# Performance work log

Hardware: AMD Instinct MI355X
Metric: run time of the kernel (lower is better)

## Reference

```python
import jax, jax.numpy as jnp
import numpy as np

N = 50000          # nodes
E = 800000         # random edges (self loops added in forward)
F_IN = 64; F_HID = 64; F_OUT = 16; H = 2  # from layers=[64,64,64,16], heads=[2,2,2]
NEG_SLOPE = 0.2    # PyG GATConv default

def _glorot(key, shape):
    fan_in, fan_out = shape[0], shape[-1]
    lim = np.sqrt(6.0 / (fan_in + fan_out)).astype(np.float32)
    return jax.random.uniform(key, shape, jnp.float32, -lim, lim)

def gat_conv(x, src, dst, W, a_src, a_dst, b, concat):
    """PyG-style GATConv: gather -> attention logits -> segment softmax -> scatter-add."""
    n = x.shape[0]
    Hh, Ff = a_src.shape
    h = (x @ W).reshape(n, Hh, Ff)                      # [N,H,F]
    al_s = jnp.sum(h * a_src[None], axis=-1)            # [N,H]
    al_d = jnp.sum(h * a_dst[None], axis=-1)            # [N,H]
    e = jax.nn.leaky_relu(al_s[src] + al_d[dst], NEG_SLOPE)  # [Etot,H]
    emax = jax.ops.segment_max(e, dst, num_segments=n)       # [N,H]
    ex = jnp.exp(e - emax[dst])
    denom = jax.ops.segment_sum(ex, dst, num_segments=n)
    alpha = ex / (denom[dst] + 1e-16)                   # softmax over in-edges of dst
    out = jax.ops.segment_sum(h[src] * alpha[:, :, None], dst, num_segments=n)  # [N,H,F]
    out = out.reshape(n, Hh * Ff) if concat else out.mean(axis=1)
    return out + b

def setup_inputs() -> dict:
    key = jax.random.key(0)
    k = jax.random.split(key, 12)
    inp = {}
    inp["feat_matrix"] = jax.random.normal(k[0], (N, F_IN), jnp.float32)
    inp["edge_index"] = jax.random.randint(k[1], (2, E), 0, N, dtype=jnp.int32)
    inp["W1"] = _glorot(k[2], (F_IN, H * F_HID))
    inp["a1_src"] = _glorot(k[3], (H, F_HID)); inp["a1_dst"] = _glorot(k[4], (H, F_HID))
    inp["b1"] = jnp.zeros((H * F_HID,), jnp.float32)
    inp["W2"] = _glorot(k[5], (H * F_HID, H * F_HID))
    inp["a2_src"] = _glorot(k[6], (H, F_HID)); inp["a2_dst"] = _glorot(k[7], (H, F_HID))
    inp["b2"] = jnp.zeros((H * F_HID,), jnp.float32)
    inp["W3"] = _glorot(k[8], (H * F_HID, H * F_OUT))
    inp["a3_src"] = _glorot(k[9], (H, F_OUT)); inp["a3_dst"] = _glorot(k[10], (H, F_OUT))
    inp["b3"] = jnp.zeros((F_OUT,), jnp.float32)
    # unused forward args of the original module
    inp["get_item_index"] = 0; inp["set_index"] = 0; inp["val_index"] = 0; inp["mask_matrix"] = 0
    return inp

def reference(feat_matrix, edge_index, W1, a1_src, a1_dst, b1, W2, a2_src, a2_dst, b2,
              W3, a3_src, a3_dst, b3, get_item_index, set_index, val_index, mask_matrix):
    loops = jnp.arange(N, dtype=edge_index.dtype)
    src = jnp.concatenate([edge_index[0], loops])   # add_self_loops=True (PyG default)
    dst = jnp.concatenate([edge_index[1], loops])
    x = jax.nn.relu(gat_conv(feat_matrix, src, dst, W1, a1_src, a1_dst, b1, True))
    x = jax.nn.relu(gat_conv(x, src, dst, W2, a2_src, a2_dst, b2, True))
    x = gat_conv(x, src, dst, W3, a3_src, a3_dst, b3, False)
    return jax.nn.softmax(x, axis=-1)
```

## Files before the change

### kernel.cpp

```cpp
#include <hip/hip_runtime.h>
#include <hip/hip_fp16.h>

#define NEG_SLOPE 0.2f

__device__ __forceinline__ float lrelu(float x) { return x > 0.f ? x : NEG_SLOPE * x; }

template<int K, int OUT, int F, bool HSPLIT>
__global__ __launch_bounds__(256) void gemm_logits(
    const float* __restrict__ X, const float* __restrict__ W,
    const float* __restrict__ a_s, const float* __restrict__ a_d,
    float* __restrict__ HoutF, __half* __restrict__ HoutH,
    float* __restrict__ als, float* __restrict__ ald,
    int n)
{
    constexpr int TX = OUT / 4;
    constexpr int TY = 256 / TX;
    constexpr int MR = 8;
    constexpr int BM = TY * MR;
    constexpr int KC = 32;

    __shared__ __align__(16) float Xs[BM][KC];
    __shared__ __align__(16) float Ws[KC][OUT];

    const int tx = (int)threadIdx.x % TX;
    const int ty = (int)threadIdx.x / TX;
    const int r0 = blockIdx.x * BM;

    float4 acc[MR];
#pragma unroll
    for (int m = 0; m < MR; ++m) acc[m] = make_float4(0.f, 0.f, 0.f, 0.f);

    for (int kc = 0; kc < K; kc += KC) {
        __syncthreads();
        constexpr int XV = BM * KC / 4;
#pragma unroll
        for (int i = threadIdx.x; i < XV; i += 256) {
            int f = i * 4;
            int r = f / KC, k = f % KC;
            int gr = r0 + r;
            float4 v = make_float4(0.f, 0.f, 0.f, 0.f);
            if (gr < n) v = *(const float4*)(X + (size_t)gr * K + kc + k);
            *(float4*)(&Xs[r][k]) = v;
        }
        constexpr int WV = KC * OUT / 4;
#pragma unroll
        for (int i = threadIdx.x; i < WV; i += 256) {
            int f = i * 4;
            int k = f / OUT, c = f % OUT;
            *(float4*)(&Ws[k][c]) = *(const float4*)(W + (size_t)(kc + k) * OUT + c);
        }
        __syncthreads();

#pragma unroll
        for (int k4 = 0; k4 < KC; k4 += 4) {
            float4 xv[MR];
#pragma unroll
            for (int m = 0; m < MR; ++m)
                xv[m] = *(const float4*)(&Xs[ty * MR + m][k4]);
#pragma unroll
            for (int kk = 0; kk < 4; ++kk) {
                float4 wv = *(const float4*)(&Ws[k4 + kk][tx * 4]);
#pragma unroll
                for (int m = 0; m < MR; ++m) {
                    float xm = kk == 0 ? xv[m].x : kk == 1 ? xv[m].y : kk == 2 ? xv[m].z : xv[m].w;
                    acc[m].x = fmaf(xm, wv.x, acc[m].x);
                    acc[m].y = fmaf(xm, wv.y, acc[m].y);
                    acc[m].z = fmaf(xm, wv.z, acc[m].z);
                    acc[m].w = fmaf(xm, wv.w, acc[m].w);
                }
            }
        }
    }

    const float4 asv = *(const float4*)(a_s + tx * 4);
    const float4 adv = *(const float4*)(a_d + tx * 4);
    constexpr int UH = F / 4;
    const int head = tx / UH;
#pragma unroll
    for (int m = 0; m < MR; ++m) {
        int gr = r0 + ty * MR + m;
        float ps = acc[m].x * asv.x + acc[m].y * asv.y + acc[m].z * asv.z + acc[m].w * asv.w;
        float pd = acc[m].x * adv.x + acc[m].y * adv.y + acc[m].z * adv.z + acc[m].w * adv.w;
#pragma unroll
        for (int off = UH / 2; off > 0; off >>= 1) {
            ps += __shfl_xor(ps, off, 64);
            pd += __shfl_xor(pd, off, 64);
        }
        if (gr < n) {
            if (HSPLIT) {
                union { __half h[4]; uint2 u; } pk;
                pk.h[0] = __float2half_rn(acc[m].x);
                pk.h[1] = __float2half_rn(acc[m].y);
                pk.h[2] = __float2half_rn(acc[m].z);
                pk.h[3] = __float2half_rn(acc[m].w);
                *(uint2*)(HoutH + ((size_t)head * n + gr) * F + (tx % UH) * 4) = pk.u;
            } else {
                *(float4*)(HoutF + (size_t)gr * OUT + tx * 4) = acc[m];
            }
            if ((tx % UH) == 0) {
                als[(size_t)head * n + gr] = ps;
                ald[(size_t)head * n + gr] = pd;
            }
        }
    }
}

#define SCAN_TILE 1024

__global__ __launch_bounds__(256) void k_zero_int(int* __restrict__ p, int n) {
    int i = blockIdx.x * 256 + threadIdx.x;
    if (i < n) p[i] = 0;
}

__global__ __launch_bounds__(256) void k_hist(const int* __restrict__ dst,
                                              int* __restrict__ deg, int E) {
    int e = blockIdx.x * 256 + threadIdx.x;
    if (e < E) atomicAdd(&deg[dst[e]], 1);
}

__global__ __launch_bounds__(256) void k_scan1(const int* __restrict__ deg,
                                               int* __restrict__ bsum, int N) {
    __shared__ int sm[256];
    int base = blockIdx.x * SCAN_TILE;
    int t = threadIdx.x;
    int s = 0;
#pragma unroll
    for (int j = 0; j < SCAN_TILE / 256; ++j) {
        int i = base + j * 256 + t;
        if (i < N) s += deg[i];
    }
    sm[t] = s;
    __syncthreads();
    for (int off = 128; off > 0; off >>= 1) {
        if (t < off) sm[t] += sm[t + off];
        __syncthreads();
    }
    if (t == 0) bsum[blockIdx.x] = sm[0];
}

__global__ __launch_bounds__(256) void k_scan3(const int* __restrict__ deg,
                                               const int* __restrict__ bsum,
                                               int* __restrict__ rowptr,
                                               int* __restrict__ cursor,
                                               int nb, int N) {
    __shared__ int sm[256];
    __shared__ int sme[256];
    int t = threadIdx.x;
    int v = (t < nb) ? bsum[t] : 0;
    sm[t] = v;
    __syncthreads();
    for (int off = 1; off < 256; off <<= 1) {
        int u = (t >= off) ? sm[t - off] : 0;
        __syncthreads();
        sm[t] += u;
        __syncthreads();
    }
    sme[t] = sm[t] - v;
    if (blockIdx.x == 0 && t == 255) rowptr[N] = sm[255];
    __syncthreads();
    const int boffv = sme[blockIdx.x];

    int base = blockIdx.x * SCAN_TILE;
    int i0 = base + t * 4;
    int d0 = 0, d1 = 0, d2 = 0, d3 = 0;
    if (i0 + 3 < N) {
        int4 dv = *(const int4*)(deg + i0);
        d0 = dv.x; d1 = dv.y; d2 = dv.z; d3 = dv.w;
    } else {
        if (i0 + 0 < N) d0 = deg[i0 + 0];
        if (i0 + 1 < N) d1 = deg[i0 + 1];
        if (i0 + 2 < N) d2 = deg[i0 + 2];
        if (i0 + 3 < N) d3 = deg[i0 + 3];
    }
    int tsum = d0 + d1 + d2 + d3;
    __syncthreads();
    sm[t] = tsum;
    __syncthreads();
    for (int off = 1; off < 256; off <<= 1) {
        int u = (t >= off) ? sm[t - off] : 0;
        __syncthreads();
        sm[t] += u;
        __syncthreads();
    }
    int run = boffv + sm[t] - tsum;
    if (i0 + 0 < N) { rowptr[i0 + 0] = run; cursor[i0 + 0] = run; run += d0; }
    if (i0 + 1 < N) { rowptr[i0 + 1] = run; cursor[i0 + 1] = run; run += d1; }
    if (i0 + 2 < N) { rowptr[i0 + 2] = run; cursor[i0 + 2] = run; run += d2; }
    if (i0 + 3 < N) { rowptr[i0 + 3] = run; cursor[i0 + 3] = run; run += d3; }
}

__global__ __launch_bounds__(256) void k_scatter_xcd(
    const int* __restrict__ src, const int* __restrict__ dst,
    int* __restrict__ cursor, int* __restrict__ esorted, int E, int chunk) {
    const int slice = blockIdx.x & 7;
    const int lo = slice * chunk;
    const int hi = lo + chunk;
    int e = (blockIdx.x >> 3) * 256 + threadIdx.x;
    if (e >= E) return;
    int d = dst[e];
    if (d < lo || d >= hi) return;
    int p = atomicAdd(&cursor[d], 1);
    esorted[p] = src[e];
}

__global__ __launch_bounds__(256) void gat_gather_head(
    const int* __restrict__ rowptr, const int* __restrict__ esorted,
    const float* __restrict__ als, const float* __restrict__ ald,
    const __half* __restrict__ Hh, const float* __restrict__ bias,
    float* __restrict__ out, int N, int nblk)
{
    const int head = (blockIdx.x >= nblk) ? 1 : 0;
    const int nodeblk = blockIdx.x - head * nblk;
    const int node = nodeblk * 16 + ((int)threadIdx.x >> 4);
    const int lane = (int)threadIdx.x & 15;
    if (node >= N) return;

    const float* __restrict__ alsh = als + (size_t)head * N;
    const float aldh = ald[(size_t)head * N + node];
    const __half* __restrict__ Ht = Hh + (size_t)head * N * 64;

    const float ws = __expf(lrelu(alsh[node] + aldh));

    uint2 uo = *(const uint2*)(Ht + (size_t)node * 64 + lane * 4);
    float2 o01 = __half22float2(*reinterpret_cast<const __half2*>(&uo.x));
    float2 o23 = __half22float2(*reinterpret_cast<const __half2*>(&uo.y));
    float4 accA = make_float4(ws * o01.x, ws * o01.y, ws * o23.x, ws * o23.y);
    float4 accB = make_float4(0.f, 0.f, 0.f, 0.f);
    float4 accC = make_float4(0.f, 0.f, 0.f, 0.f);
    float4 accD = make_float4(0.f, 0.f, 0.f, 0.f);
    float den = ws;

    int p = rowptr[node];
    const int end = rowptr[node + 1];
    for (; p + 4 <= end; p += 4) {
        int s0 = esorted[p], s1 = esorted[p + 1], s2 = esorted[p + 2], s3 = esorted[p + 3];
        float l0 = alsh[s0], l1 = alsh[s1], l2 = alsh[s2], l3 = alsh[s3];
        uint2 u0 = *(const uint2*)(Ht + (size_t)s0 * 64 + lane * 4);
        uint2 u1 = *(const uint2*)(Ht + (size_t)s1 * 64 + lane * 4);
        uint2 u2 = *(const uint2*)(Ht + (size_t)s2 * 64 + lane * 4);
        uint2 u3 = *(const uint2*)(Ht + (size_t)s3 * 64 + lane * 4);
        float w0 = __expf(lrelu(l0 + aldh));
        float w1 = __expf(lrelu(l1 + aldh));
        float w2 = __expf(lrelu(l2 + aldh));
        float w3 = __expf(lrelu(l3 + aldh));
        float2 a01 = __half22float2(*reinterpret_cast<const __half2*>(&u0.x));
        float2 a23 = __half22float2(*reinterpret_cast<const __half2*>(&u0.y));
        float2 b01 = __half22float2(*reinterpret_cast<const __half2*>(&u1.x));
        float2 b23 = __half22float2(*reinterpret_cast<const __half2*>(&u1.y));
        float2 c01 = __half22float2(*reinterpret_cast<const __half2*>(&u2.x));
        float2 c23 = __half22float2(*reinterpret_cast<const __half2*>(&u2.y));
        float2 d01 = __half22float2(*reinterpret_cast<const __half2*>(&u3.x));
        float2 d23 = __half22float2(*reinterpret_cast<const __half2*>(&u3.y));
        accA.x = fmaf(w0, a01.x, accA.x); accA.y = fmaf(w0, a01.y, accA.y);
        accA.z = fmaf(w0, a23.x, accA.z); accA.w = fmaf(w0, a23.y, accA.w);
        accB.x = fmaf(w1, b01.x, accB.x); accB.y = fmaf(w1, b01.y, accB.y);
        accB.z = fmaf(w1, b23.x, accB.z); accB.w = fmaf(w1, b23.y, accB.w);
        accC.x = fmaf(w2, c01.x, accC.x); accC.y = fmaf(w2, c01.y, accC.y);
        accC.z = fmaf(w2, c23.x, accC.z); accC.w = fmaf(w2, c23.y, accC.w);
        accD.x = fmaf(w3, d01.x, accD.x); accD.y = fmaf(w3, d01.y, accD.y);
        accD.z = fmaf(w3, d23.x, accD.z); accD.w = fmaf(w3, d23.y, accD.w);
        den += (w0 + w1) + (w2 + w3);
    }
    for (; p < end; ++p) {
        int s0 = esorted[p];
        float w0 = __expf(lrelu(alsh[s0] + aldh));
        uint2 u0 = *(const uint2*)(Ht + (size_t)s0 * 64 + lane * 4);
        float2 a01 = __half22float2(*reinterpret_cast<const __half2*>(&u0.x));
        float2 a23 = __half22float2(*reinterpret_cast<const __half2*>(&u0.y));
        accA.x = fmaf(w0, a01.x, accA.x); accA.y = fmaf(w0, a01.y, accA.y);
        accA.z = fmaf(w0, a23.x, accA.z); accA.w = fmaf(w0, a23.y, accA.w);
        den += w0;
    }

    const float r = 1.f / (den + 1e-16f);
    const float4 bv = *(const float4*)(bias + head * 64 + lane * 4);
    float4 v;
    v.x = (accA.x + accB.x + accC.x + accD.x) * r + bv.x;
    v.y = (accA.y + accB.y + accC.y + accD.y) * r + bv.y;
    v.z = (accA.z + accB.z + accC.z + accD.z) * r + bv.z;
    v.w = (accA.w + accB.w + accC.w + accD.w) * r + bv.w;
    v.x = v.x > 0.f ? v.x : 0.f;
    v.y = v.y > 0.f ? v.y : 0.f;
    v.z = v.z > 0.f ? v.z : 0.f;
    v.w = v.w > 0.f ? v.w : 0.f;
    *(float4*)(out + (size_t)node * 128 + head * 64 + lane * 4) = v;
}

__global__ __launch_bounds__(256) void gat_gather_final(
    const int* __restrict__ rowptr, const int* __restrict__ esorted,
    const float* __restrict__ als, const float* __restrict__ ald,
    const float* __restrict__ H3, const float* __restrict__ b3,
    float* __restrict__ out, int N)
{
    const int node = blockIdx.x * 32 + ((int)threadIdx.x >> 3);
    const int lane = (int)threadIdx.x & 7;
    if (node >= N) return;
    const int head = lane >> 2;
    const int sub = lane & 3;

    const float* __restrict__ alsh = als + (size_t)head * N;
    const float aldh = ald[(size_t)head * N + node];
    const float ws = __expf(lrelu(alsh[node] + aldh));

    const float4 hown = *(const float4*)(H3 + (size_t)node * 32 + head * 16 + sub * 4);
    float4 accA = make_float4(ws * hown.x, ws * hown.y, ws * hown.z, ws * hown.w);
    float4 accB = make_float4(0.f, 0.f, 0.f, 0.f);
    float den = ws;

    int p = rowptr[node];
    const int end = rowptr[node + 1];
    for (; p + 2 <= end; p += 2) {
        int s0 = esorted[p], s1 = esorted[p + 1];
        float l0 = alsh[s0], l1 = alsh[s1];
        float4 h0 = *(const float4*)(H3 + (size_t)s0 * 32 + head * 16 + sub * 4);
        float4 h1 = *(const float4*)(H3 + (size_t)s1 * 32 + head * 16 + sub * 4);
        float w0 = __expf(lrelu(l0 + aldh));
        float w1 = __expf(lrelu(l1 + aldh));
        accA.x = fmaf(w0, h0.x, accA.x); accA.y = fmaf(w0, h0.y, accA.y);
        accA.z = fmaf(w0, h0.z, accA.z); accA.w = fmaf(w0, h0.w, accA.w);
        accB.x = fmaf(w1, h1.x, accB.x); accB.y = fmaf(w1, h1.y, accB.y);
        accB.z = fmaf(w1, h1.z, accB.z); accB.w = fmaf(w1, h1.w, accB.w);
        den += w0 + w1;
    }
    if (p < end) {
        int s0 = esorted[p];
        float4 h0 = *(const float4*)(H3 + (size_t)s0 * 32 + head * 16 + sub * 4);
        float w0 = __expf(lrelu(alsh[s0] + aldh));
        accA.x = fmaf(w0, h0.x, accA.x); accA.y = fmaf(w0, h0.y, accA.y);
        accA.z = fmaf(w0, h0.z, accA.z); accA.w = fmaf(w0, h0.w, accA.w);
        den += w0;
    }

    const float r = 1.f / (den + 1e-16f);
    float4 a;
    a.x = (accA.x + accB.x) * r;
    a.y = (accA.y + accB.y) * r;
    a.z = (accA.z + accB.z) * r;
    a.w = (accA.w + accB.w) * r;
    float4 ap;
    ap.x = __shfl_xor(a.x, 4, 64);
    ap.y = __shfl_xor(a.y, 4, 64);
    ap.z = __shfl_xor(a.z, 4, 64);
    ap.w = __shfl_xor(a.w, 4, 64);
    const float4 bv = *(const float4*)(b3 + sub * 4);
    float4 v;
    v.x = 0.5f * (a.x + ap.x) + bv.x;
    v.y = 0.5f * (a.y + ap.y) + bv.y;
    v.z = 0.5f * (a.z + ap.z) + bv.z;
    v.w = 0.5f * (a.w + ap.w) + bv.w;
    float mx = fmaxf(fmaxf(v.x, v.y), fmaxf(v.z, v.w));
    mx = fmaxf(mx, __shfl_xor(mx, 1, 64));
    mx = fmaxf(mx, __shfl_xor(mx, 2, 64));
    float4 ex;
    ex.x = expf(v.x - mx);
    ex.y = expf(v.y - mx);
    ex.z = expf(v.z - mx);
    ex.w = expf(v.w - mx);
    float sum = ex.x + ex.y + ex.z + ex.w;
    sum += __shfl_xor(sum, 1, 64);
    sum += __shfl_xor(sum, 2, 64);
    const float rs = 1.f / sum;
    if (head == 0) {
        float4 o = make_float4(ex.x * rs, ex.y * rs, ex.z * rs, ex.w * rs);
        *(float4*)(out + (size_t)node * 16 + sub * 4) = o;
    }
}

extern "C" void kernel_launch(void* const* d_in, const int* in_sizes, int n_in,
                              void* d_out, int out_size, void* d_ws, size_t ws_size,
                              hipStream_t stream)
{
    const float* feat = (const float*)d_in[0];
    const int*   ei   = (const int*)d_in[1];
    const float* W1 = (const float*)d_in[2];
    const float* a1s = (const float*)d_in[3];
    const float* a1d = (const float*)d_in[4];
    const float* b1 = (const float*)d_in[5];
    const float* W2 = (const float*)d_in[6];
    const float* a2s = (const float*)d_in[7];
    const float* a2d = (const float*)d_in[8];
    const float* b2 = (const float*)d_in[9];
    const float* W3 = (const float*)d_in[10];
    const float* a3s = (const float*)d_in[11];
    const float* a3d = (const float*)d_in[12];
    const float* b3 = (const float*)d_in[13];

    const int N = in_sizes[0] / 64;
    const int E = in_sizes[1] / 2;
    const int* src = ei;
    const int* dst = ei + E;
    const int n2 = N * 2;
    const int nb = (N + SCAN_TILE - 1) / SCAN_TILE;

    float* bufA  = (float*)d_ws;
    float* bufB  = bufA + (size_t)N * 128;
    float* als   = bufB + (size_t)N * 128;
    float* ald   = als + (size_t)n2;
    int* deg     = (int*)(ald + (size_t)n2);
    int* rowptr  = deg + N;
    int* cursor  = rowptr + (N + 1);
    int* bsum    = cursor + N;
    int* esorted = bsum + nb;
    __half* HhA  = (__half*)bufA;

    dim3 blk(256);
    const int gE = (E + 255) / 256;
    const int nblk16 = (N + 15) / 16;
    const int chunk = (N + 7) / 8;

    k_zero_int<<<(N + 255) / 256, blk, 0, stream>>>(deg, N);
    k_hist<<<gE, blk, 0, stream>>>(dst, deg, E);
    k_scan1<<<nb, blk, 0, stream>>>(deg, bsum, N);
    k_scan3<<<nb, blk, 0, stream>>>(deg, bsum, rowptr, cursor, nb, N);
    k_scatter_xcd<<<8 * gE, blk, 0, stream>>>(src, dst, cursor, esorted, E, chunk);

    gemm_logits<64, 128, 64, true><<<(N + 63) / 64, blk, 0, stream>>>(
        feat, W1, a1s, a1d, nullptr, HhA, als, ald, N);
    gat_gather_head<<<2 * nblk16, blk, 0, stream>>>(rowptr, esorted, als, ald, HhA, b1, bufB, N, nblk16);

    gemm_logits<128, 128, 64, true><<<(N + 63) / 64, blk, 0, stream>>>(
        bufB, W2, a2s, a2d, nullptr, HhA, als, ald, N);
    gat_gather_head<<<2 * nblk16, blk, 0, stream>>>(rowptr, esorted, als, ald, HhA, b2, bufB, N, nblk16);

    gemm_logits<128, 32, 16, false><<<(N + 255) / 256, blk, 0, stream>>>(
        bufB, W3, a3s, a3d, bufA, nullptr, als, ald, N);
    gat_gather_final<<<(N + 31) / 32, blk, 0, stream>>>(rowptr, esorted, als, ald, bufA, b3, (float*)d_out, N);
}
```

Baseline: 259.8 us.

## Use fp16 MFMA matrix cores for the 128-wide GAT projection GEMMs

Adds a new GEMM kernel that converts X and W tiles to fp16 in shared memory and computes layers 1 and 2 with 16x16x32 f16 MFMA instructions, fusing the attention-logit dot products and the per-head fp16 output. It replaces the scalar FP32 tiled GEMM for those layers, aiming to cut GEMM compute time. Inputs are rounded to fp16 before the multiply, which lowers precision relative to the fp32 GEMM. The output stores are scalar half writes with a strided pattern, which may hurt coalescing.

```diff
diff --git a/kernel.cpp b/kernel.cpp
--- a/kernel.cpp
+++ b/kernel.cpp
@@ -5,12 +5,109 @@
 
 __device__ __forceinline__ float lrelu(float x) { return x > 0.f ? x : NEG_SLOPE * x; }
 
-template<int K, int OUT, int F, bool HSPLIT>
+using half8 = __attribute__((ext_vector_type(8))) _Float16;
+using f32x4 = __attribute__((ext_vector_type(4))) float;
+
+template<int K>
+__global__ __launch_bounds__(256) void gemm_mfma128(
+    const float* __restrict__ X, const float* __restrict__ W,
+    const float* __restrict__ a_s, const float* __restrict__ a_d,
+    __half* __restrict__ HoutH, float* __restrict__ als, float* __restrict__ ald,
+    int n)
+{
+    constexpr int KP = K + 8;
+    __shared__ __align__(16) _Float16 Xs[64 * KP];
+    __shared__ __align__(16) _Float16 Wt[128 * KP];
+
+    const int tid = (int)threadIdx.x;
+    const int wid = tid >> 6;
+    const int lane = tid & 63;
+    const int r0 = blockIdx.x * 64;
+
+    for (int i = tid; i < 64 * K / 4; i += 256) {
+        int r = i / (K / 4);
+        int kc = (i % (K / 4)) * 4;
+        int gr = r0 + r;
+        float4 v = make_float4(0.f, 0.f, 0.f, 0.f);
+        if (gr < n) v = *(const float4*)(X + (size_t)gr * K + kc);
+        _Float16* d = &Xs[r * KP + kc];
+        d[0] = (_Float16)v.x; d[1] = (_Float16)v.y;
+        d[2] = (_Float16)v.z; d[3] = (_Float16)v.w;
+    }
+    for (int i = tid; i < K * 128 / 4; i += 256) {
+        int k = i / 32;
+        int c = (i % 32) * 4;
+        float4 v = *(const float4*)(W + (size_t)k * 128 + c);
+        Wt[(c + 0) * KP + k] = (_Float16)v.x;
+        Wt[(c + 1) * KP + k] = (_Float16)v.y;
+        Wt[(c + 2) * KP + k] = (_Float16)v.z;
+        Wt[(c + 3) * KP + k] = (_Float16)v.w;
+    }
+    __syncthreads();
+
+    const int arow = wid * 16 + (lane & 15);
+    const int kg = (lane >> 4) * 8;
+
+    f32x4 acc[8];
+#pragma unroll
+    for (int ct = 0; ct < 8; ++ct) acc[ct] = (f32x4){0.f, 0.f, 0.f, 0.f};
+
+#pragma unroll
+    for (int k0 = 0; k0 < K; k0 += 32) {
+        half8 a = *(const half8*)&Xs[arow * KP + k0 + kg];
+#pragma unroll
+        for (int ct = 0; ct < 8; ++ct) {
+            half8 b = *(const half8*)&Wt[(ct * 16 + (lane & 15)) * KP + k0 + kg];
+            acc[ct] = __builtin_amdgcn_mfma_f32_16x16x32_f16(a, b, acc[ct], 0, 0, 0);
+        }
+    }
+
+    const int ccol = lane & 15;
+    float asl[8], adl[8];
+#pragma unroll
+    for (int ct = 0; ct < 8; ++ct) {
+        asl[ct] = a_s[ct * 16 + ccol];
+        adl[ct] = a_d[ct * 16 + ccol];
+    }
+    const int crow = wid * 16 + (lane >> 4) * 4;
+
+#pragma unroll
+    for (int j = 0; j < 4; ++j) {
+        int gr = r0 + crow + j;
+        float ps0 = 0.f, pd0 = 0.f, ps1 = 0.f, pd1 = 0.f;
+#pragma unroll
+        for (int ct = 0; ct < 8; ++ct) {
+            float h = acc[ct][j];
+            if (ct < 4) { ps0 = fmaf(h, asl[ct], ps0); pd0 = fmaf(h, adl[ct], pd0); }
+            else        { ps1 = fmaf(h, asl[ct], ps1); pd1 = fmaf(h, adl[ct], pd1); }
+        }
+#pragma unroll
+        for (int off = 1; off < 16; off <<= 1) {
+            ps0 += __shfl_xor(ps0, off, 64);
+            pd0 += __shfl_xor(pd0, off, 64);
+            ps1 += __shfl_xor(ps1, off, 64);
+            pd1 += __shfl_xor(pd1, off, 64);
+        }
+        if (gr < n) {
+            if (ccol == 0) {
+                als[gr] = ps0;              ald[gr] = pd0;
+                als[(size_t)n + gr] = ps1;  ald[(size_t)n + gr] = pd1;
+            }
+#pragma unroll
+            for (int ct = 0; ct < 8; ++ct) {
+                int col = ct * 16 + ccol;
+                HoutH[((size_t)(col >> 6) * n + gr) * 64 + (col & 63)] =
+                    __float2half_rn(acc[ct][j]);
+            }
+        }
+    }
+}
+
+template<int K, int OUT, int F>
 __global__ __launch_bounds__(256) void gemm_logits(
     const float* __restrict__ X, const float* __restrict__ W,
     const float* __restrict__ a_s, const float* __restrict__ a_d,
-    float* __restrict__ HoutF, __half* __restrict__ HoutH,
-    float* __restrict__ als, float* __restrict__ ald,
+    float* __restrict__ HoutF, float* __restrict__ als, float* __restrict__ ald,
     int n)
 {
     constexpr int TX = OUT / 4;
@@ -87,16 +184,7 @@
             pd += __shfl_xor(pd, off, 64);
         }
         if (gr < n) {
-            if (HSPLIT) {
-                union { __half h[4]; uint2 u; } pk;
-                pk.h[0] = __float2half_rn(acc[m].x);
-                pk.h[1] = __float2half_rn(acc[m].y);
-                pk.h[2] = __float2half_rn(acc[m].z);
-                pk.h[3] = __float2half_rn(acc[m].w);
-                *(uint2*)(HoutH + ((size_t)head * n + gr) * F + (tx % UH) * 4) = pk.u;
-            } else {
-                *(float4*)(HoutF + (size_t)gr * OUT + tx * 4) = acc[m];
-            }
+            *(float4*)(HoutF + (size_t)gr * OUT + tx * 4) = acc[m];
             if ((tx % UH) == 0) {
                 als[(size_t)head * n + gr] = ps;
                 ald[(size_t)head * n + gr] = pd;
@@ -406,6 +494,7 @@
     dim3 blk(256);
     const int gE = (E + 255) / 256;
     const int nblk16 = (N + 15) / 16;
+    const int gM = (N + 63) / 64;
     const int chunk = (N + 7) / 8;
 
     k_zero_int<<<(N + 255) / 256, blk, 0, stream>>>(deg, N);
@@ -414,15 +503,13 @@
     k_scan3<<<nb, blk, 0, stream>>>(deg, bsum, rowptr, cursor, nb, N);
     k_scatter_xcd<<<8 * gE, blk, 0, stream>>>(src, dst, cursor, esorted, E, chunk);
 
-    gemm_logits<64, 128, 64, true><<<(N + 63) / 64, blk, 0, stream>>>(
-        feat, W1, a1s, a1d, nullptr, HhA, als, ald, N);
+    gemm_mfma128<64><<<gM, blk, 0, stream>>>(feat, W1, a1s, a1d, HhA, als, ald, N);
     gat_gather_head<<<2 * nblk16, blk, 0, stream>>>(rowptr, esorted, als, ald, HhA, b1, bufB, N, nblk16);
 
-    gemm_logits<128, 128, 64, true><<<(N + 63) / 64, blk, 0, stream>>>(
-        bufB, W2, a2s, a2d, nullptr, HhA, als, ald, N);
+    gemm_mfma128<128><<<gM, blk, 0, stream>>>(bufB, W2, a2s, a2d, HhA, als, ald, N);
     gat_gather_head<<<2 * nblk16, blk, 0, stream>>>(rowptr, esorted, als, ald, HhA, b2, bufB, N, nblk16);
 
-    gemm_logits<128, 32, 16, false><<<(N + 255) / 256, blk, 0, stream>>>(
-        bufB, W3, a3s, a3d, bufA, nullptr, als, ald, N);
+    gemm_logits<128, 32, 16><<<(N + 255) / 256, blk, 0, stream>>>(
+        bufB, W3, a3s, a3d, bufA, als, ald, N);
     gat_gather_final<<<(N + 31) / 32, blk, 0, stream>>>(rowptr, esorted, als, ald, bufA, b3, (float*)d_out, N);
 }
```

Result: faster. 250.7 us (-3.5%).
